# Optimization experiments

Measured on AMD Instinct MI355X. Metric: run time of the kernel, lower is better.

## Reference

```python
import jax, jax.numpy as jnp
import numpy as np
import math

B, L, D, H, PK = 8, 512, 1024, 16, 5
DK = D // H


def _xavier(key, shape):
    fan_in, fan_out = shape[-1], shape[-2] if len(shape) > 1 else shape[-1]
    lim = math.sqrt(6.0 / (fan_in + fan_out))
    return jax.random.uniform(key, shape, jnp.float32, -lim, lim)


def setup_inputs() -> dict:
    key = jax.random.key(0)
    ks = jax.random.split(key, 12)
    inp = {
        "src": jax.random.normal(ks[0], (B, L, D), jnp.float32),
        "tgt": jax.random.normal(ks[1], (B, L, D), jnp.float32),
        "gpm": jax.random.randint(ks[2], (B, L, L), 0, PK, jnp.int32),
        "src_mask": jnp.ones((B, L), dtype=bool),
        # shared LayerNorm params (applied to both src and tgt)
        "ln_g": jnp.ones((D,), jnp.float32),
        "ln_b": jnp.zeros((D,), jnp.float32),
        # torch Linear convention: weight [out, in], y = x @ W.T + b
        "q_w": _xavier(ks[3], (D, D)),
        "k_w": _xavier(ks[4], (D, D)),
        "v_w1": _xavier(ks[5], (D, D)),
        "v_b1": jnp.zeros((D,), jnp.float32),
        "v_w2": _xavier(ks[6], (D, D)),
        "v_b2": jnp.zeros((D,), jnp.float32),
        "rel_k": _xavier(ks[7], (PK, DK)),
        # reset_parameters: gating weight = 0, bias = 1
        "gate_w": jnp.zeros((D, D), jnp.float32),
        "gate_b": jnp.ones((D,), jnp.float32),
        "out_w": _xavier(ks[8], (D, D)),
        "out_b": jnp.zeros((D,), jnp.float32),
    }
    return inp


def _layer_norm(x, g, b, eps=1e-6):
    mu = jnp.mean(x, axis=-1, keepdims=True)
    var = jnp.var(x, axis=-1, keepdims=True)
    return (x - mu) * jax.lax.rsqrt(var + eps) * g + b


def reference(src, tgt, gpm, src_mask, ln_g, ln_b, q_w, k_w, v_w1, v_b1,
              v_w2, v_b2, rel_k, gate_w, gate_b, out_w, out_b):
    bs = src.shape[0]
    s = _layer_norm(src, ln_g, ln_b)
    t = _layer_norm(tgt, ln_g, ln_b)
    k = s @ k_w.T
    q = t @ q_w.T
    v = jax.nn.relu(t @ v_w1.T + v_b1) @ v_w2.T + v_b2  # dropout = identity (eval)
    # [B, H, L, DK]
    q1 = q.reshape(bs, -1, H, DK).transpose(0, 2, 1, 3)
    k1 = k.reshape(bs, -1, H, DK).transpose(0, 2, 1, 3)
    v1 = v.reshape(bs, -1, H, DK).transpose(0, 2, 1, 3)
    attn1 = jnp.einsum("bhid,bhjd->bhij", q1, k1)
    # relative-position bias: one-hot(gpm) @ (q1 @ rel_k.T) == gather along p
    qr = jnp.einsum("bhid,pd->bhip", q1, rel_k)            # [B,H,L,PK]
    idx = jnp.broadcast_to(gpm[:, None].astype(jnp.int32), attn1.shape)
    attn2 = jnp.take_along_axis(qr, idx, axis=-1)          # [B,H,L,L]
    attn = (attn1 + attn2) / math.sqrt(DK)
    # src_mask only (tgt_mask=None branch): mask keys
    attn = jnp.where(src_mask[:, None, None, :], attn, jnp.float32(-9e9))
    attn = jax.nn.softmax(attn, axis=-1)
    out = jnp.einsum("bhij,bhjd->bhid", attn, v1)
    out = out.transpose(0, 2, 1, 3).reshape(bs, -1, D)     # [B,L,D]
    gate = jax.nn.sigmoid(s @ gate_w.T + gate_b)
    out = (out * gate) @ out_w.T + out_b
    return out
```

## Files before the change

kernel.cpp:

```cpp
#include <hip/hip_runtime.h>
#include <hip/hip_bf16.h>


typedef unsigned short u16;
typedef __bf16 bf16x8 __attribute__((ext_vector_type(8)));
typedef float f32x4 __attribute__((ext_vector_type(4)));
typedef u16 u16x4 __attribute__((ext_vector_type(4)));
typedef u16 u16x8 __attribute__((ext_vector_type(8)));
typedef unsigned char u8x16 __attribute__((ext_vector_type(16)));

__device__ __forceinline__ float b2f(u16 u) {
  union { unsigned int i; float f; } c; c.i = ((unsigned int)u) << 16; return c.f;
}
__device__ __forceinline__ u16 f2b(float f) {
  union { __bf16 h; u16 u; } c; c.h = (__bf16)f; return c.u;
}
__device__ __forceinline__ void async_load16(const void* g, void* lds) {
  __builtin_amdgcn_global_load_lds(
      (const __attribute__((address_space(1))) void*)g,
      (__attribute__((address_space(3))) void*)lds, 16, 0, 0);
}
__device__ __forceinline__ bf16x8 lds_frag(const u16* p) {
  return *reinterpret_cast<const bf16x8*>(p);
}

__global__ __launch_bounds__(256) void prep_kernel(
    const float* __restrict__ q_w, const float* __restrict__ v_w1,
    const float* __restrict__ k_w, const float* __restrict__ gate_w,
    const float* __restrict__ v_w2, const float* __restrict__ out_w,
    const int* __restrict__ gpm, const float* __restrict__ src,
    const float* __restrict__ tgt, const float* __restrict__ ln_g,
    const float* __restrict__ ln_b, u16* __restrict__ wout,
    unsigned char* __restrict__ gateNZ, u16* __restrict__ s_out,
    u16* __restrict__ t_out, unsigned char* __restrict__ gpmP) {
  __shared__ float red[8];
  __shared__ unsigned int rnz;
  const int bid = blockIdx.x;
  const int t = threadIdx.x;

  if (bid < 6144) {
    int w = bid >> 10;
    int idx = (bid & 1023) * 256 + t;
    const float* sp = (w == 0) ? q_w : (w == 1) ? v_w1 : (w == 2) ? k_w
                     : (w == 3) ? gate_w : (w == 4) ? v_w2 : out_w;
    f32x4 v = reinterpret_cast<const f32x4*>(sp)[idx];
    if (w == 3) {
      if (t == 0) rnz = 0u;
      __syncthreads();
      bool nz = (v[0] != 0.f) || (v[1] != 0.f) || (v[2] != 0.f) || (v[3] != 0.f);
      if (__any(nz)) { if ((t & 63) == 0) atomicOr(&rnz, 1u); }
      __syncthreads();
      if (t == 0) gateNZ[bid & 1023] = (unsigned char)rnz;
    }
    u16x4 o;
#pragma unroll
    for (int e = 0; e < 4; ++e) o[e] = f2b(v[e]);
    reinterpret_cast<u16x4*>(wout + ((size_t)w << 20))[idx] = o;
    return;
  }

  if (bid < 6400) {
    int bx = bid - 6144;
    int kvt = bx & 7, qt = (bx >> 3) & 3, b = bx >> 5;
    const int* g = gpm + (size_t)b * 512 * 512;
#pragma unroll
    for (int half = 0; half < 2; ++half) {
      int tt = t + half * 256;
      int lane = tt & 63, wv = tt >> 6;
      int rbase = qt * 128 + wv * 16 + ((lane >> 4) << 2);
      int cbase = kvt * 64 + (lane & 15);
      u8x16 v;
#pragma unroll
      for (int fj = 0; fj < 4; ++fj)
#pragma unroll
        for (int j4 = 0; j4 < 4; ++j4)
          v[fj * 4 + j4] = (unsigned char)g[(rbase + j4) * 512 + cbase + fj * 16];
      reinterpret_cast<u8x16*>(gpmP)[(size_t)bx * 512 + tt] = v;
    }
    return;
  }

  int row = bid - 6400;
  const float* x; u16* y;
  if (row < 4096) { x = src + (size_t)row * 1024; y = s_out + (size_t)row * 1024; }
  else { x = tgt + (size_t)(row - 4096) * 1024; y = t_out + (size_t)(row - 4096) * 1024; }
  f32x4 f = *reinterpret_cast<const f32x4*>(x + t * 4);
  float s1 = 0.f, s2 = 0.f;
#pragma unroll
  for (int e = 0; e < 4; ++e) { s1 += f[e]; s2 += f[e] * f[e]; }
#pragma unroll
  for (int off = 32; off > 0; off >>= 1) { s1 += __shfl_down(s1, off); s2 += __shfl_down(s2, off); }
  int wv = t >> 6;
  if ((t & 63) == 0) { red[wv] = s1; red[wv + 4] = s2; }
  __syncthreads();
  float tot1 = red[0] + red[1] + red[2] + red[3];
  float tot2 = red[4] + red[5] + red[6] + red[7];
  float mean = tot1 * (1.f / 1024.f);
  float var = tot2 * (1.f / 1024.f) - mean * mean;
  float rs = rsqrtf(var + 1e-6f);
  f32x4 g = *reinterpret_cast<const f32x4*>(ln_g + t * 4);
  f32x4 b = *reinterpret_cast<const f32x4*>(ln_b + t * 4);
  u16x4 o;
#pragma unroll
  for (int e = 0; e < 4; ++e) o[e] = f2b((f[e] - mean) * rs * g[e] + b[e]);
  *(u16x4*)(y + t * 4) = o;
}

#define GEMM_BODY(APTR, WPTR)                                                  \
  f32x4 acc[4][4] = {};                                                        \
  for (int kt = 0; kt < 1024; kt += 64) {                                      \
    _Pragma("unroll")                                                          \
    for (int cc = 0; cc < 4; ++cc) {                                           \
      int rblk = wid * 4 + cc;                                                 \
      int r = rblk * 8 + (lane >> 3);                                          \
      int c = lane & 7;                                                        \
      int sk = kt + ((c ^ (r & 7)) << 3);                                      \
      async_load16(APTR + (size_t)(arow0 + r) * 1024 + sk, &As[rblk * 512]);   \
      async_load16(WPTR + (size_t)(col0 + r) * 1024 + sk, &Bs[rblk * 512]);    \
    }                                                                          \
    __syncthreads();                                                           \
    _Pragma("unroll")                                                          \
    for (int ks = 0; ks < 2; ++ks) {                                           \
      bf16x8 af[4], bfr[4];                                                    \
      _Pragma("unroll")                                                        \
      for (int m = 0; m < 4; ++m) {                                            \
        int r = wr + m * 16 + (lane & 15);                                     \
        int ch = (ks * 4 + (lane >> 4)) ^ (r & 7);                             \
        af[m] = lds_frag(&As[r * 64 + ch * 8]);                                \
      }                                                                        \
      _Pragma("unroll")                                                        \
      for (int n = 0; n < 4; ++n) {                                            \
        int r = wc + n * 16 + (lane & 15);                                     \
        int ch = (ks * 4 + (lane >> 4)) ^ (r & 7);                             \
        bfr[n] = lds_frag(&Bs[r * 64 + ch * 8]);                               \
      }                                                                        \
      _Pragma("unroll")                                                        \
      for (int m = 0; m < 4; ++m)                                              \
        _Pragma("unroll")                                                      \
        for (int n = 0; n < 4; ++n)                                            \
          acc[m][n] = __builtin_amdgcn_mfma_f32_16x16x32_bf16(                 \
              af[m], bfr[n], acc[m][n], 0, 0, 0);                              \
    }                                                                          \
    __syncthreads();                                                           \
  }

__global__ __launch_bounds__(256, 4) void gemm_mega(
    const u16* __restrict__ A, const u16* __restrict__ w_kg,
    const u16* __restrict__ w_qv, const float* __restrict__ gate_b,
    const float* __restrict__ v_b1, const unsigned char* __restrict__ gateNZ,
    u16* __restrict__ Kb, u16* __restrict__ Gate, u16* __restrict__ Qb,
    u16* __restrict__ Vmid) {
  const int bid = blockIdx.x;
  const int xcd = bid & 7, w = bid >> 3;
  const int arow0 = (xcd + 8 * (w & 7)) * 128;
  const int col0 = (w >> 3) * 128;
  const int tid = threadIdx.x, lane = tid & 63, wid = tid >> 6;
  const bool th = arow0 >= 4096;
  const int row0 = arow0 & 4095;
  const bool hi = col0 >= 1024;
  const int cb = col0 & 1023;
  const int wr = (wid >> 1) * 64, wc = (wid & 1) * 64;

  __shared__ unsigned int gnz;
  if (tid == 0) gnz = 0u;
  __syncthreads();
  if (!th && hi && tid < 32) {
    unsigned int v = reinterpret_cast<const unsigned int*>(gateNZ + cb)[tid];
    if (v) atomicOr(&gnz, 1u);
  }
  __syncthreads();

  if (!th && hi && gnz == 0u) {
    float bv[4];
#pragma unroll
    for (int n = 0; n < 4; ++n) {
      float bb = gate_b[cb + wc + n * 16 + (lane & 15)];
      bv[n] = 1.f / (1.f + __expf(-bb));
    }
#pragma unroll
    for (int m = 0; m < 4; ++m) {
      int rbase = wr + m * 16 + (lane >> 4) * 4;
#pragma unroll
      for (int n = 0; n < 4; ++n) {
        int c = cb + wc + n * 16 + (lane & 15);
        u16 ov = f2b(bv[n]);
#pragma unroll
        for (int j = 0; j < 4; ++j)
          Gate[(size_t)(row0 + rbase + j) * 1024 + c] = ov;
      }
    }
    return;
  }

  __shared__ u16 As[128 * 64];
  __shared__ u16 Bs[128 * 64];
  const u16* W = th ? w_qv : w_kg;
  GEMM_BODY(A, W)

  float bv[4];
  if (hi) {
    const float* bias = th ? v_b1 : gate_b;
#pragma unroll
    for (int n = 0; n < 4; ++n) bv[n] = bias[cb + wc + n * 16 + (lane & 15)];
  }
  u16* out = th ? (hi ? Vmid : Qb) : (hi ? Gate : Kb);
#pragma unroll
  for (int m = 0; m < 4; ++m) {
    int rbase = wr + m * 16 + (lane >> 4) * 4;
#pragma unroll
    for (int n = 0; n < 4; ++n) {
      int c = cb + wc + n * 16 + (lane & 15);
#pragma unroll
      for (int j = 0; j < 4; ++j) {
        float v = acc[m][n][j];
        if (hi) {
          v += bv[n];
          v = th ? fmaxf(v, 0.f) : 1.f / (1.f + __expf(-v));
        }
        out[(size_t)(row0 + rbase + j) * 1024 + c] = f2b(v);
      }
    }
  }
}

__global__ __launch_bounds__(256, 2) void vtqr_kernel(
    const u16* __restrict__ A, const u16* __restrict__ W,
    const float* __restrict__ bias, u16* __restrict__ vt,
    const u16* __restrict__ qb, const float* __restrict__ relk,
    float* __restrict__ qrAll) {
  __shared__ u16 As[64 * 64];
  __shared__ u16 Bs[128 * 64];
  const int gbid = blockIdx.x;
  const int tid = threadIdx.x, lane = tid & 63, wid = tid >> 6;

  if (gbid >= 512) {
    constexpr float SCL = 0.125f * 1.4426950408889634f;
    int bx = gbid - 512;
    const int h = bx & 15, qt = (bx >> 4) & 3, b = bx >> 6;
    for (int idx = tid; idx < 640; idx += 256) {
      int i = idx & 127, p = idx >> 7;
      const u16* qp = qb + ((size_t)(b * 512 + qt * 128 + i)) * 1024 + h * 64;
      const float* rk = relk + p * 64;
      float a = 0.f;
#pragma unroll
      for (int c = 0; c < 8; ++c) {
        u16x8 v8 = *(const u16x8*)(qp + c * 8);
#pragma unroll
        for (int e = 0; e < 8; ++e) a += b2f(v8[e]) * rk[c * 8 + e];
      }
      qrAll[(size_t)bx * 1024 + i * 8 + p] = a * SCL;
    }
    return;
  }

  const int bid = gbid;
  const int xcd = bid & 7, w = bid >> 3;
  const int arow0 = (xcd * 8 + (w & 7)) * 64;
  const int col0 = (w >> 3) * 128;
  const int wr = (wid >> 1) * 32, wc = (wid & 1) * 64;
  f32x4 acc[2][4] = {};

  for (int kt = 0; kt < 1024; kt += 64) {
    {
      int c = lane & 7;
#pragma unroll
      for (int cc = 0; cc < 2; ++cc) {
        int rblk = wid * 2 + cc;
        int r = rblk * 8 + (lane >> 3);
        int sk = kt + ((c ^ (r & 7)) << 3);
        async_load16(A + (size_t)(arow0 + r) * 1024 + sk, &As[rblk * 512]);
      }
#pragma unroll
      for (int cc = 0; cc < 4; ++cc) {
        int rblk = wid * 4 + cc;
        int r = rblk * 8 + (lane >> 3);
        int sk = kt + ((c ^ (r & 7)) << 3);
        async_load16(W + (size_t)(col0 + r) * 1024 + sk, &Bs[rblk * 512]);
      }
    }
    __syncthreads();
#pragma unroll
    for (int ks = 0; ks < 2; ++ks) {
      bf16x8 af[2], bfr[4];
#pragma unroll
      for (int m = 0; m < 2; ++m) {
        int r = wr + m * 16 + (lane & 15);
        int ch = (ks * 4 + (lane >> 4)) ^ (r & 7);
        af[m] = lds_frag(&As[r * 64 + ch * 8]);
      }
#pragma unroll
      for (int n = 0; n < 4; ++n) {
        int r = wc + n * 16 + (lane & 15);
        int ch = (ks * 4 + (lane >> 4)) ^ (r & 7);
        bfr[n] = lds_frag(&Bs[r * 64 + ch * 8]);
      }
#pragma unroll
      for (int m = 0; m < 2; ++m)
#pragma unroll
        for (int n = 0; n < 4; ++n)
          acc[m][n] = __builtin_amdgcn_mfma_f32_16x16x32_bf16(
              af[m], bfr[n], acc[m][n], 0, 0, 0);
    }
    __syncthreads();
  }

  float bv[4];
#pragma unroll
  for (int n = 0; n < 4; ++n) bv[n] = bias[col0 + wc + n * 16 + (lane & 15)];
#pragma unroll
  for (int m = 0; m < 2; ++m) {
    int rbase = wr + m * 16 + (lane >> 4) * 4;
#pragma unroll
    for (int n = 0; n < 4; ++n) {
      int c = col0 + wc + n * 16 + (lane & 15);
      int grow0 = arow0 + rbase;
      int bb = grow0 >> 9, jj0 = grow0 & 511;
      int hh = c >> 6, dd = c & 63;
      u16x4 ov;
#pragma unroll
      for (int j = 0; j < 4; ++j) ov[j] = f2b(acc[m][n][j] + bv[n]);
      *reinterpret_cast<u16x4*>(
          vt + (((size_t)(bb * 16 + hh) * 64) + dd) * 512 + jj0) = ov;
    }
  }
}

__global__ __launch_bounds__(256, 2) void gemm64_out(
    const u16* __restrict__ A, const u16* __restrict__ W,
    const float* __restrict__ bias, float* __restrict__ Cout) {
  const int bid = blockIdx.x;
  const int xcd = bid & 7, w = bid >> 3;
  const int arow0 = (xcd * 8 + (w & 7)) * 64;
  const int col0 = (w >> 3) * 128;
  __shared__ u16 As[64 * 64];
  __shared__ u16 Bs[128 * 64];
  const int tid = threadIdx.x, lane = tid & 63, wid = tid >> 6;
  const int wr = (wid >> 1) * 32, wc = (wid & 1) * 64;
  f32x4 acc[2][4] = {};

  for (int kt = 0; kt < 1024; kt += 64) {
    {
      int c = lane & 7;
#pragma unroll
      for (int cc = 0; cc < 2; ++cc) {
        int rblk = wid * 2 + cc;
        int r = rblk * 8 + (lane >> 3);
        int sk = kt + ((c ^ (r & 7)) << 3);
        async_load16(A + (size_t)(arow0 + r) * 1024 + sk, &As[rblk * 512]);
      }
#pragma unroll
      for (int cc = 0; cc < 4; ++cc) {
        int rblk = wid * 4 + cc;
        int r = rblk * 8 + (lane >> 3);
        int sk = kt + ((c ^ (r & 7)) << 3);
        async_load16(W + (size_t)(col0 + r) * 1024 + sk, &Bs[rblk * 512]);
      }
    }
    __syncthreads();
#pragma unroll
    for (int ks = 0; ks < 2; ++ks) {
      bf16x8 af[2], bfr[4];
#pragma unroll
      for (int m = 0; m < 2; ++m) {
        int r = wr + m * 16 + (lane & 15);
        int ch = (ks * 4 + (lane >> 4)) ^ (r & 7);
        af[m] = lds_frag(&As[r * 64 + ch * 8]);
      }
#pragma unroll
      for (int n = 0; n < 4; ++n) {
        int r = wc + n * 16 + (lane & 15);
        int ch = (ks * 4 + (lane >> 4)) ^ (r & 7);
        bfr[n] = lds_frag(&Bs[r * 64 + ch * 8]);
      }
#pragma unroll
      for (int m = 0; m < 2; ++m)
#pragma unroll
        for (int n = 0; n < 4; ++n)
          acc[m][n] = __builtin_amdgcn_mfma_f32_16x16x32_bf16(
              af[m], bfr[n], acc[m][n], 0, 0, 0);
    }
    __syncthreads();
  }

  float bv[4];
#pragma unroll
  for (int n = 0; n < 4; ++n) bv[n] = bias[col0 + wc + n * 16 + (lane & 15)];
#pragma unroll
  for (int m = 0; m < 2; ++m) {
    int rbase = wr + m * 16 + (lane >> 4) * 4;
#pragma unroll
    for (int n = 0; n < 4; ++n) {
      int c = col0 + wc + n * 16 + (lane & 15);
#pragma unroll
      for (int j = 0; j < 4; ++j)
        Cout[(size_t)(arow0 + rbase + j) * 1024 + c] = acc[m][n][j] + bv[n];
    }
  }
}

__global__ __launch_bounds__(512, 2) void attn_kernel(
    const u16* __restrict__ qb, const u16* __restrict__ kb,
    const u16* __restrict__ vtb, const u16* __restrict__ gateb,
    const unsigned char* __restrict__ gpmP, const float* __restrict__ qrAll,
    u16* __restrict__ gated) {
  constexpr int L = 512, D = 1024;
  constexpr float SCL = 0.125f * 1.4426950408889634f;
  constexpr float THR = 8.f;
  __shared__ u16 Ks[64 * 64];
  __shared__ u16 VTs[64 * 64];
  __shared__ u16 Ps[8][16 * 64];
  __shared__ float qr_s[128][8];
  const int tid = threadIdx.x, lane = tid & 63, wid = tid >> 6;
  const int bx = blockIdx.x;
  const int h = bx & 15, qt = (bx >> 4) & 3, b = bx >> 6;

  const int r0 = wid * 8 + (lane >> 3);
  const int sw0 = (((lane & 7) ^ (r0 & 7)) << 3);
  const u16* kbase = kb + ((size_t)(b * L)) * D + h * 64;
  const u16* vbase = vtb + ((size_t)((b * 16 + h) * 64)) * L;

  async_load16(kbase + (size_t)r0 * D + sw0, &Ks[wid * 512]);
  async_load16(vbase + (size_t)r0 * L + sw0, &VTs[wid * 512]);

  bf16x8 qf[2];
  {
    int qi = qt * 128 + wid * 16 + (lane & 15);
    const u16* qrow = qb + ((size_t)(b * L + qi)) * D + h * 64 + (lane >> 4) * 8;
    qf[0] = *(const bf16x8*)(qrow);
    qf[1] = *(const bf16x8*)(qrow + 32);
  }
  if (tid < 256) {
    f32x4 v = reinterpret_cast<const f32x4*>(qrAll + (size_t)bx * 1024)[tid];
    reinterpret_cast<f32x4*>(&qr_s[0][0])[tid] = v;
  }

  f32x4 accO[4] = {};
  float m_run[4], l_run[4];
#pragma unroll
  for (int j4 = 0; j4 < 4; ++j4) { m_run[j4] = -1e30f; l_run[j4] = 0.f; }
  __syncthreads();

  const int ib0 = wid * 16 + (lane >> 4) * 4;
  const u8x16* gpp = reinterpret_cast<const u8x16*>(gpmP) +
                     ((size_t)(b * 4 + qt)) * 8 * 512;
  u8x16 pv = gpp[tid];
  for (int t = 0; t < 8; ++t) {
    u16x8 kst, vst;
    u8x16 pvn;
    if (t < 7) {
      int kvn = (t + 1) * 64;
      kst = *(const u16x8*)(kbase + (size_t)(kvn + r0) * D + sw0);
      vst = *(const u16x8*)(vbase + (size_t)r0 * L + kvn + sw0);
      pvn = gpp[(t + 1) * 512 + tid];
    }

    f32x4 sacc[4] = {};
    __builtin_amdgcn_s_setprio(1);
#pragma unroll
    for (int ks = 0; ks < 2; ++ks)
#pragma unroll
      for (int fj = 0; fj < 4; ++fj) {
        int jr = fj * 16 + (lane & 15);
        int ch = (ks * 4 + (lane >> 4)) ^ (jr & 7);
        bf16x8 kf = lds_frag(&Ks[jr * 64 + ch * 8]);
        sacc[fj] = __builtin_amdgcn_mfma_f32_16x16x32_bf16(qf[ks], kf, sacc[fj], 0, 0, 0);
      }
    __builtin_amdgcn_s_setprio(0);

    float mt[4] = {-1e30f, -1e30f, -1e30f, -1e30f};
#pragma unroll
    for (int fj = 0; fj < 4; ++fj)
#pragma unroll
      for (int j4 = 0; j4 < 4; ++j4) {
        int p = pv[fj * 4 + j4];
        float sv = fmaf(sacc[fj][j4], SCL, qr_s[ib0 + j4][p]);
        sacc[fj][j4] = sv;
        mt[j4] = fmaxf(mt[j4], sv);
      }
#pragma unroll
    for (int off = 1; off < 16; off <<= 1)
#pragma unroll
      for (int j4 = 0; j4 < 4; ++j4) mt[j4] = fmaxf(mt[j4], __shfl_xor(mt[j4], off));

    bool over = (mt[0] > m_run[0] + THR) || (mt[1] > m_run[1] + THR) ||
                (mt[2] > m_run[2] + THR) || (mt[3] > m_run[3] + THR);
    if (__any(over)) {
      float sc[4];
#pragma unroll
      for (int j4 = 0; j4 < 4; ++j4) {
        float mn = fmaxf(m_run[j4], mt[j4]);
        sc[j4] = exp2f(m_run[j4] - mn);
        m_run[j4] = mn;
        l_run[j4] *= sc[j4];
      }
#pragma unroll
      for (int n = 0; n < 4; ++n)
#pragma unroll
        for (int j4 = 0; j4 < 4; ++j4) accO[n][j4] *= sc[j4];
    }

    float ts[4] = {0.f, 0.f, 0.f, 0.f};
#pragma unroll
    for (int fj = 0; fj < 4; ++fj)
#pragma unroll
      for (int j4 = 0; j4 < 4; ++j4) {
        float e = exp2f(sacc[fj][j4] - m_run[j4]);
        sacc[fj][j4] = e;
        ts[j4] += e;
      }
#pragma unroll
    for (int off = 1; off < 16; off <<= 1)
#pragma unroll
      for (int j4 = 0; j4 < 4; ++j4) ts[j4] += __shfl_xor(ts[j4], off);
#pragma unroll
    for (int j4 = 0; j4 < 4; ++j4) l_run[j4] += ts[j4];

    u16* Pw = Ps[wid];
#pragma unroll
    for (int fj = 0; fj < 4; ++fj) {
      int jl = fj * 16 + (lane & 15);
      int chl = jl >> 3;
#pragma unroll
      for (int j4 = 0; j4 < 4; ++j4) {
        int iw = (lane >> 4) * 4 + j4;
        int ch = chl ^ (iw & 7);
        Pw[iw * 64 + ch * 8 + (jl & 7)] = f2b(sacc[fj][j4]);
      }
    }

    __builtin_amdgcn_s_setprio(1);
#pragma unroll
    for (int ks2 = 0; ks2 < 2; ++ks2) {
      int i = lane & 15;
      int ch = (ks2 * 4 + (lane >> 4)) ^ (i & 7);
      bf16x8 pf = lds_frag(&Pw[i * 64 + ch * 8]);
#pragma unroll
      for (int n = 0; n < 4; ++n) {
        int dcol = n * 16 + (lane & 15);
        int vch = (ks2 * 4 + (lane >> 4)) ^ (dcol & 7);
        bf16x8 vf = lds_frag(&VTs[dcol * 64 + vch * 8]);
        accO[n] = __builtin_amdgcn_mfma_f32_16x16x32_bf16(pf, vf, accO[n], 0, 0, 0);
      }
    }
    __builtin_amdgcn_s_setprio(0);

    __syncthreads();
    if (t < 7) {
      *(u16x8*)(&Ks[wid * 512 + lane * 8]) = kst;
      *(u16x8*)(&VTs[wid * 512 + lane * 8]) = vst;
      __syncthreads();
      pv = pvn;
    }
  }

#pragma unroll
  for (int n = 0; n < 4; ++n)
#pragma unroll
    for (int j4 = 0; j4 < 4; ++j4) {
      int ib = ib0 + j4;
      size_t gi = (size_t)(b * L + qt * 128 + ib);
      int d = h * 64 + n * 16 + (lane & 15);
      float ov = accO[n][j4] / l_run[j4];
      float ga = b2f(gateb[gi * D + d]);
      gated[gi * D + d] = f2b(ov * ga);
    }
}

extern "C" void kernel_launch(void* const* d_in, const int* in_sizes, int n_in,
                              void* d_out, int out_size, void* d_ws, size_t ws_size,
                              hipStream_t stream) {
  const float* src  = (const float*)d_in[0];
  const float* tgt  = (const float*)d_in[1];
  const int*   gpm  = (const int*)d_in[2];
  const float* ln_g = (const float*)d_in[4];
  const float* ln_b = (const float*)d_in[5];
  const float* q_w  = (const float*)d_in[6];
  const float* k_w  = (const float*)d_in[7];
  const float* v_w1 = (const float*)d_in[8];
  const float* v_b1 = (const float*)d_in[9];
  const float* v_w2 = (const float*)d_in[10];
  const float* v_b2 = (const float*)d_in[11];
  const float* relk = (const float*)d_in[12];
  const float* gate_w = (const float*)d_in[13];
  const float* gate_b = (const float*)d_in[14];
  const float* out_w  = (const float*)d_in[15];
  const float* out_b  = (const float*)d_in[16];

  u16* ws = (u16*)d_ws;
  const size_t M1 = (size_t)1 << 20;
  u16* wcat_qv = ws;
  u16* wcat_kg = ws + 2 * M1;
  u16* wv2     = ws + 4 * M1;
  u16* wo      = ws + 5 * M1;
  const size_t T = (size_t)4096 * 1024;
  u16* Ss   = ws + 6 * M1;
  u16* Tt   = ws + 6 * M1 + 1 * T;
  u16* Qb   = ws + 6 * M1 + 2 * T;
  u16* Kb   = ws + 6 * M1 + 3 * T;
  u16* Vmid = ws + 6 * M1 + 4 * T;
  u16* Gate = ws + 6 * M1 + 5 * T;
  unsigned char* gpmP = (unsigned char*)(ws + 6 * M1 + 6 * T);
  float* qrAll = (float*)(gpmP + 2 * 1024 * 1024);
  unsigned char* gateNZ = (unsigned char*)(qrAll + 524288);

  prep_kernel<<<14592, 256, 0, stream>>>(q_w, v_w1, k_w, gate_w, v_w2, out_w,
                                         gpm, src, tgt, ln_g, ln_b,
                                         ws, gateNZ, Ss, Tt, gpmP);

  gemm_mega<<<1024, 256, 0, stream>>>(Ss, wcat_kg, wcat_qv, gate_b, v_b1,
                                      gateNZ, Kb, Gate, Qb, Vmid);
  vtqr_kernel<<<1024, 256, 0, stream>>>(Vmid, wv2, v_b2, Ss, Qb, relk, qrAll);
  attn_kernel<<<512, 512, 0, stream>>>(Qb, Kb, Ss, Gate, gpmP, qrAll, Tt);
  gemm64_out<<<512, 256, 0, stream>>>(Tt, wo, out_b, (float*)d_out);
}
```

Before: 129.8 us.

## Widen attention KV tile to 128 keys and repack gpm to match

The attention kernel now processes 128 keys per iteration instead of 64, cutting the loop from 8 to 4 steps and halving the barriers and online-softmax rescale checks. K, V^T and P shared-memory buffers double, and the prep kernel repacks the gpm position indices into 32-byte chunks per thread to match the new tile. This costs more registers (8 score fragments) and more LDS per block, which may lower occupancy under the 512-thread, 2-block launch bound.

```diff
diff --git a/kernel.cpp b/kernel.cpp
--- a/kernel.cpp
+++ b/kernel.cpp
@@ -59,28 +59,32 @@
     return;
   }
 
-  if (bid < 6400) {
+  if (bid < 6272) {
     int bx = bid - 6144;
-    int kvt = bx & 7, qt = (bx >> 3) & 3, b = bx >> 5;
+    int kvt = bx & 3, qt = (bx >> 2) & 3, b = bx >> 4;
     const int* g = gpm + (size_t)b * 512 * 512;
 #pragma unroll
     for (int half = 0; half < 2; ++half) {
       int tt = t + half * 256;
       int lane = tt & 63, wv = tt >> 6;
       int rbase = qt * 128 + wv * 16 + ((lane >> 4) << 2);
-      int cbase = kvt * 64 + (lane & 15);
-      u8x16 v;
+      int cbase = kvt * 128 + (lane & 15);
+      u8x16 v0, v1;
 #pragma unroll
       for (int fj = 0; fj < 4; ++fj)
 #pragma unroll
-        for (int j4 = 0; j4 < 4; ++j4)
-          v[fj * 4 + j4] = (unsigned char)g[(rbase + j4) * 512 + cbase + fj * 16];
-      reinterpret_cast<u8x16*>(gpmP)[(size_t)bx * 512 + tt] = v;
+        for (int j4 = 0; j4 < 4; ++j4) {
+          v0[fj * 4 + j4] = (unsigned char)g[(rbase + j4) * 512 + cbase + fj * 16];
+          v1[fj * 4 + j4] = (unsigned char)g[(rbase + j4) * 512 + cbase + (fj + 4) * 16];
+        }
+      u8x16* dst = reinterpret_cast<u8x16*>(gpmP + ((size_t)bx * 512 + tt) * 32);
+      dst[0] = v0;
+      dst[1] = v1;
     }
     return;
   }
 
-  int row = bid - 6400;
+  int row = bid - 6272;
   const float* x; u16* y;
   if (row < 4096) { x = src + (size_t)row * 1024; y = s_out + (size_t)row * 1024; }
   else { x = tgt + (size_t)(row - 4096) * 1024; y = t_out + (size_t)(row - 4096) * 1024; }
@@ -406,21 +410,27 @@
   constexpr int L = 512, D = 1024;
   constexpr float SCL = 0.125f * 1.4426950408889634f;
   constexpr float THR = 8.f;
-  __shared__ u16 Ks[64 * 64];
-  __shared__ u16 VTs[64 * 64];
-  __shared__ u16 Ps[8][16 * 64];
+  __shared__ u16 Ks[128 * 64];
+  __shared__ u16 VTs[64 * 128];
+  __shared__ u16 Ps[8][16 * 128];
   __shared__ float qr_s[128][8];
   const int tid = threadIdx.x, lane = tid & 63, wid = tid >> 6;
   const int bx = blockIdx.x;
   const int h = bx & 15, qt = (bx >> 4) & 3, b = bx >> 6;
 
-  const int r0 = wid * 8 + (lane >> 3);
-  const int sw0 = (((lane & 7) ^ (r0 & 7)) << 3);
+  const int kr0 = wid * 16 + (lane >> 3), kr1 = kr0 + 8;
+  const int ksw0 = (((lane & 7) ^ (kr0 & 7)) << 3);
+  const int ksw1 = (((lane & 7) ^ (kr1 & 7)) << 3);
+  const int vd0 = wid * 8 + (lane >> 4), vd1 = vd0 + 4;
+  const int vsw0 = (((lane & 15) ^ (vd0 & 7)) << 3);
+  const int vsw1 = (((lane & 15) ^ (vd1 & 7)) << 3);
   const u16* kbase = kb + ((size_t)(b * L)) * D + h * 64;
   const u16* vbase = vtb + ((size_t)((b * 16 + h) * 64)) * L;
 
-  async_load16(kbase + (size_t)r0 * D + sw0, &Ks[wid * 512]);
-  async_load16(vbase + (size_t)r0 * L + sw0, &VTs[wid * 512]);
+  async_load16(kbase + (size_t)kr0 * D + ksw0, &Ks[wid * 1024]);
+  async_load16(kbase + (size_t)kr1 * D + ksw1, &Ks[wid * 1024 + 512]);
+  async_load16(vbase + (size_t)vd0 * L + vsw0, &VTs[wid * 1024]);
+  async_load16(vbase + (size_t)vd1 * L + vsw1, &VTs[wid * 1024 + 512]);
 
   bf16x8 qf[2];
   {
@@ -441,25 +451,28 @@
   __syncthreads();
 
   const int ib0 = wid * 16 + (lane >> 4) * 4;
-  const u8x16* gpp = reinterpret_cast<const u8x16*>(gpmP) +
-                     ((size_t)(b * 4 + qt)) * 8 * 512;
-  u8x16 pv = gpp[tid];
-  for (int t = 0; t < 8; ++t) {
-    u16x8 kst, vst;
-    u8x16 pvn;
-    if (t < 7) {
-      int kvn = (t + 1) * 64;
-      kst = *(const u16x8*)(kbase + (size_t)(kvn + r0) * D + sw0);
-      vst = *(const u16x8*)(vbase + (size_t)r0 * L + kvn + sw0);
-      pvn = gpp[(t + 1) * 512 + tid];
-    }
-
-    f32x4 sacc[4] = {};
+  const u8x16* gpp = reinterpret_cast<const u8x16*>(
+      gpmP + ((size_t)(b * 4 + qt)) * 4 * 512 * 32);
+  u8x16 pv0 = gpp[tid * 2], pv1 = gpp[tid * 2 + 1];
+  for (int t = 0; t < 4; ++t) {
+    u16x8 kst0, kst1, vst0, vst1;
+    u8x16 pvn0, pvn1;
+    if (t < 3) {
+      int kvn = (t + 1) * 128;
+      kst0 = *(const u16x8*)(kbase + (size_t)(kvn + kr0) * D + ksw0);
+      kst1 = *(const u16x8*)(kbase + (size_t)(kvn + kr1) * D + ksw1);
+      vst0 = *(const u16x8*)(vbase + (size_t)vd0 * L + kvn + vsw0);
+      vst1 = *(const u16x8*)(vbase + (size_t)vd1 * L + kvn + vsw1);
+      pvn0 = gpp[((t + 1) * 512 + tid) * 2];
+      pvn1 = gpp[((t + 1) * 512 + tid) * 2 + 1];
+    }
+
+    f32x4 sacc[8] = {};
     __builtin_amdgcn_s_setprio(1);
 #pragma unroll
     for (int ks = 0; ks < 2; ++ks)
 #pragma unroll
-      for (int fj = 0; fj < 4; ++fj) {
+      for (int fj = 0; fj < 8; ++fj) {
         int jr = fj * 16 + (lane & 15);
         int ch = (ks * 4 + (lane >> 4)) ^ (jr & 7);
         bf16x8 kf = lds_frag(&Ks[jr * 64 + ch * 8]);
@@ -469,10 +482,10 @@
 
     float mt[4] = {-1e30f, -1e30f, -1e30f, -1e30f};
 #pragma unroll
-    for (int fj = 0; fj < 4; ++fj)
+    for (int fj = 0; fj < 8; ++fj)
 #pragma unroll
       for (int j4 = 0; j4 < 4; ++j4) {
-        int p = pv[fj * 4 + j4];
+        int p = (fj < 4) ? pv0[fj * 4 + j4] : pv1[(fj - 4) * 4 + j4];
         float sv = fmaf(sacc[fj][j4], SCL, qr_s[ib0 + j4][p]);
         sacc[fj][j4] = sv;
         mt[j4] = fmaxf(mt[j4], sv);
@@ -501,7 +514,7 @@
 
     float ts[4] = {0.f, 0.f, 0.f, 0.f};
 #pragma unroll
-    for (int fj = 0; fj < 4; ++fj)
+    for (int fj = 0; fj < 8; ++fj)
 #pragma unroll
       for (int j4 = 0; j4 < 4; ++j4) {
         float e = exp2f(sacc[fj][j4] - m_run[j4]);
@@ -517,39 +530,41 @@
 
     u16* Pw = Ps[wid];
 #pragma unroll
-    for (int fj = 0; fj < 4; ++fj) {
+    for (int fj = 0; fj < 8; ++fj) {
       int jl = fj * 16 + (lane & 15);
       int chl = jl >> 3;
 #pragma unroll
       for (int j4 = 0; j4 < 4; ++j4) {
         int iw = (lane >> 4) * 4 + j4;
         int ch = chl ^ (iw & 7);
-        Pw[iw * 64 + ch * 8 + (jl & 7)] = f2b(sacc[fj][j4]);
+        Pw[iw * 128 + ch * 8 + (jl & 7)] = f2b(sacc[fj][j4]);
       }
     }
 
     __builtin_amdgcn_s_setprio(1);
 #pragma unroll
-    for (int ks2 = 0; ks2 < 2; ++ks2) {
+    for (int ks2 = 0; ks2 < 4; ++ks2) {
       int i = lane & 15;
       int ch = (ks2 * 4 + (lane >> 4)) ^ (i & 7);
-      bf16x8 pf = lds_frag(&Pw[i * 64 + ch * 8]);
+      bf16x8 pf = lds_frag(&Pw[i * 128 + ch * 8]);
 #pragma unroll
       for (int n = 0; n < 4; ++n) {
         int dcol = n * 16 + (lane & 15);
         int vch = (ks2 * 4 + (lane >> 4)) ^ (dcol & 7);
-        bf16x8 vf = lds_frag(&VTs[dcol * 64 + vch * 8]);
+        bf16x8 vf = lds_frag(&VTs[dcol * 128 + vch * 8]);
         accO[n] = __builtin_amdgcn_mfma_f32_16x16x32_bf16(pf, vf, accO[n], 0, 0, 0);
       }
     }
     __builtin_amdgcn_s_setprio(0);
 
     __syncthreads();
-    if (t < 7) {
-      *(u16x8*)(&Ks[wid * 512 + lane * 8]) = kst;
-      *(u16x8*)(&VTs[wid * 512 + lane * 8]) = vst;
+    if (t < 3) {
+      *(u16x8*)(&Ks[wid * 1024 + lane * 8]) = kst0;
+      *(u16x8*)(&Ks[wid * 1024 + 512 + lane * 8]) = kst1;
+      *(u16x8*)(&VTs[wid * 1024 + lane * 8]) = vst0;
+      *(u16x8*)(&VTs[wid * 1024 + 512 + lane * 8]) = vst1;
       __syncthreads();
-      pv = pvn;
+      pv0 = pvn0; pv1 = pvn1;
     }
   }
 
@@ -603,7 +618,7 @@
   float* qrAll = (float*)(gpmP + 2 * 1024 * 1024);
   unsigned char* gateNZ = (unsigned char*)(qrAll + 524288);
 
-  prep_kernel<<<14592, 256, 0, stream>>>(q_w, v_w1, k_w, gate_w, v_w2, out_w,
+  prep_kernel<<<14464, 256, 0, stream>>>(q_w, v_w1, k_w, gate_w, v_w2, out_w,
                                          gpm, src, tgt, ln_g, ln_b,
                                          ws, gateNZ, Ss, Tt, gpmP);
 
```

Result: no change. 131.1 us (+1.0%).
